# Kernel tuning notes

Measured on AMD Instinct MI355X. Metric: run time of the kernel, lower is better.

Reference implementation:

```python
import jax, jax.numpy as jnp
import numpy as np

DIM = 4096
N_HEADS = 32
N_KV = 8
HD = 128
SW = 4096          # sliding window / cache length
B = 32             # max_batch_size (decode batch)
MAX_SEQ = 8192
START_POS = 4000
CURRENT_POS = 4000

def _nearest_32(n):
    return ((n + 31) // 32) * 32

PADDED_LEN = min(_nearest_32(START_POS + 1), SW)  # 4032

def _rope_tables():
    inv_freq = 1.0 / (10000.0 ** (np.arange(0, HD, 2, dtype=np.float32) / HD))
    t = np.arange(MAX_SEQ, dtype=np.float32)
    freqs = np.outer(t, inv_freq)                       # [MAX_SEQ, HD/2]
    emb = np.concatenate([freqs, freqs], axis=-1)       # [MAX_SEQ, HD]
    return jnp.asarray(np.cos(emb)), jnp.asarray(np.sin(emb))

def rotate_half(u):
    u1, u2 = jnp.split(u, 2, axis=-1)
    return jnp.concatenate([-u2, u1], axis=-1)

def setup_inputs() -> dict:
    key = jax.random.key(0)
    ks = jax.random.split(key, 6)
    cos_cached, sin_cached = _rope_tables()
    return {
        "x": jax.random.normal(ks[0], (1, 1, B, DIM), jnp.float32),
        "wqkv": jax.random.normal(ks[1], (DIM, DIM + 2 * N_KV * HD), jnp.float32) * 0.02,
        "wo": jax.random.normal(ks[2], (DIM, DIM), jnp.float32) * 0.02,
        "cache_k": jax.random.normal(ks[3], (B, N_KV, SW, HD), jnp.float32) * 0.5,
        "cache_v": jax.random.normal(ks[4], (B, N_KV, SW, HD), jnp.float32) * 0.5,
        "cos_cached": cos_cached,
        "sin_cached": sin_cached,
        "attn_mask": jnp.zeros((B, N_HEADS, 1, PADDED_LEN), jnp.float32),
        "start_pos": START_POS,
        "current_pos": CURRENT_POS,
    }

def reference(x, wqkv, wo, cache_k, cache_v, cos_cached, sin_cached, attn_mask,
              start_pos, current_pos):
    group = N_HEADS // N_KV
    padded_len = min(_nearest_32(start_pos + 1), SW)
    scale = 1.0 / jnp.sqrt(jnp.float32(HD))

    # fused QKV projection: x (1,1,B,DIM) @ wqkv -> (B, DIM + 2*N_KV*HD)
    xqkv = x[0, 0] @ wqkv
    q = xqkv[:, :DIM].reshape(B, N_HEADS, HD)
    k = xqkv[:, DIM:DIM + N_KV * HD].reshape(B, N_KV, HD)
    v = xqkv[:, DIM + N_KV * HD:].reshape(B, N_KV, HD)

    # rotary embedding at position start_pos (single decode token)
    cos = cos_cached[start_pos]   # [HD]
    sin = sin_cached[start_pos]
    q = q * cos + rotate_half(q) * sin
    k = k * cos + rotate_half(k) * sin

    # sliding-window KV cache update at current_pos
    cache_k = cache_k.at[:, :, current_pos, :].set(k)
    cache_v = cache_v.at[:, :, current_pos, :].set(v)
    keys = cache_k[:, :, :padded_len, :]     # [B, N_KV, L, HD]
    values = cache_v[:, :, :padded_len, :]

    # grouped attention: q heads grouped by kv head
    qg = q.reshape(B, N_KV, group, HD)
    scores = jnp.einsum('bkgd,bkld->bkgl', qg, keys) * scale
    scores = scores + attn_mask.reshape(B, N_KV, group, padded_len)
    probs = jax.nn.softmax(scores, axis=-1)
    out = jnp.einsum('bkgl,bkld->bkgd', probs, values)   # [B, N_KV, group, HD]

    # concat heads and output projection
    dense = out.reshape(B, DIM) @ wo
    return dense.reshape(1, 1, B, DIM)
```

## Files before the change

### kernel.cpp

```cpp
#include <hip/hip_runtime.h>
#include <hip/hip_bf16.h>

typedef unsigned int u32;
typedef unsigned short u16;

__device__ __forceinline__ u16 f2bf(float f){ u32 x; __builtin_memcpy(&x,&f,4); u32 r=(x+0x7fffu+((x>>16)&1u))>>16; return (u16)r; }
__device__ __forceinline__ float lo2f(u32 u){ u32 x=u<<16; float f; __builtin_memcpy(&f,&x,4); return f; }
__device__ __forceinline__ float hi2f(u32 u){ u32 x=u&0xffff0000u; float f; __builtin_memcpy(&f,&x,4); return f; }

__global__ __launch_bounds__(256) void transpose_x(
    const float* __restrict__ x, float* __restrict__ xt)
{
    __shared__ float ld[32][65];
    const int t = threadIdx.x;
    const int g = blockIdx.x;
    #pragma unroll
    for (int i=0;i<8;++i) {
        const int e = i*256 + t;
        const int b = e >> 6, dd = e & 63;
        ld[b][dd] = x[(size_t)b*4096 + g*64 + dd];
    }
    __syncthreads();
    #pragma unroll
    for (int i=0;i<8;++i) {
        const int e = i*256 + t;
        const int dd = e >> 5, b = e & 31;
        xt[(size_t)(g*64 + dd)*32 + b] = ld[b][dd];
    }
}

__global__ __launch_bounds__(256) void gemm_splitk_t(
    const float* __restrict__ At, const float2* __restrict__ W2,
    float* __restrict__ P, int K, int N, int dps)
{
    const int j2 = blockIdx.x*256 + threadIdx.x;
    const int s = blockIdx.y;
    float acc0[32], acc1[32];
    #pragma unroll
    for (int b=0;b<32;++b){ acc0[b]=0.f; acc1[b]=0.f; }
    const int d0 = s*dps, d1 = d0 + dps;
    const int halfN = N >> 1;
    #pragma unroll 2
    for (int d=d0; d<d1; ++d) {
        const float2 wv = W2[(size_t)d*halfN + j2];
        const float* __restrict__ Ad = At + d*32;
        #pragma unroll
        for (int b=0;b<32;++b) {
            const float av = Ad[b];
            acc0[b] = fmaf(av, wv.x, acc0[b]);
            acc1[b] = fmaf(av, wv.y, acc1[b]);
        }
    }
    float* Pp = P + (size_t)(s*32)*N + 2*j2;
    #pragma unroll
    for (int b=0;b<32;++b)
        *reinterpret_cast<float2*>(Pp + (size_t)b*N) = make_float2(acc0[b], acc1[b]);
}

__global__ __launch_bounds__(256) void qkv_finish(
    const float* __restrict__ P, const float* __restrict__ cosc,
    const float* __restrict__ sinc, const int* __restrict__ spp,
    float* __restrict__ qws, float* __restrict__ kn, float* __restrict__ vn,
    int splits)
{
    __shared__ float sh[256];
    const int t = threadIdx.x;
    const int col = blockIdx.x*256 + t;
    const int b = blockIdx.y;
    float v = 0.f;
    for (int s=0;s<splits;++s) v += P[(size_t)(s*32+b)*6144 + col];
    sh[t] = v;
    __syncthreads();
    if (col < 5120) {
        const int d = col & 127;
        const int pt = (t & ~127) | ((d<64)? d+64 : d-64);
        const float pv = sh[pt];
        const int spos = *spp;
        const float c  = cosc[spos*128 + d];
        const float sn = sinc[spos*128 + d];
        const float rot = (d<64)? -pv : pv;
        const float val = fmaf(v, c, rot*sn);
        if (col < 4096) qws[(size_t)b*4096 + col] = val;
        else            kn[(size_t)b*1024 + (col-4096)] = val;
    } else {
        vn[(size_t)b*1024 + (col-5120)] = v;
    }
}

__global__ __launch_bounds__(1024, 4) void attn_kernel(
    const float* __restrict__ qws, const float* __restrict__ Kc,
    const float* __restrict__ Vc, const float* __restrict__ kn,
    const float* __restrict__ vn, const float* __restrict__ mask,
    const int* __restrict__ curp, float* __restrict__ aout_t,
    const int PL, const int SW)
{
    __shared__ float scoresS[4*4100];
    __shared__ float obuf[16][4][128];
    __shared__ float redm[16][4];
    __shared__ float reds[16][4];

    const int t = threadIdx.x;
    const int lane = t & 63;
    const int w = t >> 6;
    const int b  = blockIdx.x >> 3;
    const int kv = blockIdx.x & 7;
    const int cur = *curp;

    const size_t mat = (size_t)(b*8+kv);
    const float* __restrict__ Kb  = Kc + mat*(size_t)SW*128;
    const float* __restrict__ knr = kn + mat*128;
    const float* __restrict__ qbase = qws + (size_t)(b*32 + kv*4)*128;

    const int l   = lane & 15;
    const int grp = lane >> 4;
    float qv[4][8];
    #pragma unroll
    for (int h=0;h<4;++h)
        #pragma unroll
        for (int j=0;j<8;++j)
            qv[h][j] = qbase[h*128 + l*8 + j];

    const int rpw = PL >> 4;
    const int rb0 = w * rpw;
    for (int g=0; g<rpw; g+=4) {
        const int r = rb0 + g + grp;
        const float* __restrict__ row = (r==cur) ? knr : (Kb + (size_t)r*128);
        const float4 ka = *reinterpret_cast<const float4*>(row + l*8);
        const float4 kb4 = *reinterpret_cast<const float4*>(row + l*8 + 4);
        float kf[8];
        kf[0]=ka.x; kf[1]=ka.y; kf[2]=ka.z; kf[3]=ka.w;
        kf[4]=kb4.x; kf[5]=kb4.y; kf[6]=kb4.z; kf[7]=kb4.w;
        float sc0=0.f, sc1=0.f, sc2=0.f, sc3=0.f;
        #pragma unroll
        for (int j=0;j<8;++j) {
            sc0 = fmaf(qv[0][j], kf[j], sc0);
            sc1 = fmaf(qv[1][j], kf[j], sc1);
            sc2 = fmaf(qv[2][j], kf[j], sc2);
            sc3 = fmaf(qv[3][j], kf[j], sc3);
        }
        #pragma unroll
        for (int off=8; off; off>>=1) {
            sc0 += __shfl_xor(sc0, off, 16);
            sc1 += __shfl_xor(sc1, off, 16);
            sc2 += __shfl_xor(sc2, off, 16);
            sc3 += __shfl_xor(sc3, off, 16);
        }
        if (l < 4) {
            const float v = (l==0)?sc0:(l==1)?sc1:(l==2)?sc2:sc3;
            scoresS[l*4100 + r] = v;
        }
    }
    __syncthreads();

    const float scale = 0.08838834764831845f;
    const size_t mbase = ((size_t)b*32 + (size_t)kv*4)*(size_t)PL;
    const float* __restrict__ Vb  = Vc + mat*(size_t)SW*128;
    const float* __restrict__ vnr = vn + mat*128;
    const int chunk = PL >> 4;
    const int p0 = w*chunk, p1 = p0 + chunk;

    float m0=-3.0e38f, m1=-3.0e38f, m2=-3.0e38f, m3=-3.0e38f;
    float l0=0.f, l1=0.f, l2=0.f, l3=0.f;
    float a0[4] = {0.f,0.f,0.f,0.f}, a1[4] = {0.f,0.f,0.f,0.f};

    #pragma unroll 4
    for (int p=p0; p<p1; ++p) {
        const float* row = (p==cur) ? vnr : (Vb + (size_t)p*128);
        const float2 vv = *reinterpret_cast<const float2*>(row + 2*lane);

        const float sc0 = fmaf(scoresS[         p], scale, mask[mbase              + p]);
        const float sc1 = fmaf(scoresS[ 4100 +  p], scale, mask[mbase +   (size_t)PL + p]);
        const float sc2 = fmaf(scoresS[ 8200 +  p], scale, mask[mbase + 2*(size_t)PL + p]);
        const float sc3 = fmaf(scoresS[12300 +  p], scale, mask[mbase + 3*(size_t)PL + p]);

        const float n0 = fmaxf(m0, sc0), n1 = fmaxf(m1, sc1);
        const float n2 = fmaxf(m2, sc2), n3 = fmaxf(m3, sc3);
        const float f0 = __expf(m0 - n0), f1 = __expf(m1 - n1);
        const float f2 = __expf(m2 - n2), f3 = __expf(m3 - n3);
        const float e0 = __expf(sc0 - n0), e1 = __expf(sc1 - n1);
        const float e2 = __expf(sc2 - n2), e3 = __expf(sc3 - n3);
        m0 = n0; m1 = n1; m2 = n2; m3 = n3;
        l0 = fmaf(l0, f0, e0); l1 = fmaf(l1, f1, e1);
        l2 = fmaf(l2, f2, e2); l3 = fmaf(l3, f3, e3);

        a0[0] = fmaf(e0, vv.x, a0[0]*f0); a1[0] = fmaf(e0, vv.y, a1[0]*f0);
        a0[1] = fmaf(e1, vv.x, a0[1]*f1); a1[1] = fmaf(e1, vv.y, a1[1]*f1);
        a0[2] = fmaf(e2, vv.x, a0[2]*f2); a1[2] = fmaf(e2, vv.y, a1[2]*f2);
        a0[3] = fmaf(e3, vv.x, a0[3]*f3); a1[3] = fmaf(e3, vv.y, a1[3]*f3);
    }

    if (lane==0) {
        redm[w][0]=m0; redm[w][1]=m1; redm[w][2]=m2; redm[w][3]=m3;
        reds[w][0]=l0; reds[w][1]=l1; reds[w][2]=l2; reds[w][3]=l3;
    }
    #pragma unroll
    for (int h=0;h<4;++h)
        *reinterpret_cast<float2*>(&obuf[w][h][2*lane]) = make_float2(a0[h], a1[h]);
    __syncthreads();

    if (t < 512) {
        const int h = t >> 7;
        const int d = t & 127;
        float M = redm[0][h];
        #pragma unroll
        for (int ww=1;ww<16;++ww) M = fmaxf(M, redm[ww][h]);
        float num = 0.f, den = 0.f;
        #pragma unroll
        for (int ww=0;ww<16;++ww) {
            const float f = __expf(redm[ww][h] - M);
            num = fmaf(f, obuf[ww][h][d], num);
            den = fmaf(f, reds[ww][h], den);
        }
        const int col = (kv*4 + h)*128 + d;
        aout_t[(size_t)col*32 + b] = num/den;
    }
}

__global__ __launch_bounds__(256) void wo_finish(
    const float* __restrict__ P, float* __restrict__ out, int splits)
{
    const int col = blockIdx.x*256 + threadIdx.x;
    const int b = blockIdx.y;
    float v = 0.f;
    for (int s=0;s<splits;++s) v += P[(size_t)(s*32+b)*4096 + col];
    out[(size_t)b*4096 + col] = v;
}

extern "C" void kernel_launch(void* const* d_in, const int* in_sizes, int n_in,
                              void* d_out, int out_size, void* d_ws, size_t ws_size,
                              hipStream_t stream)
{
    const float* x    = (const float*)d_in[0];
    const float* wqkv = (const float*)d_in[1];
    const float* wo   = (const float*)d_in[2];
    const float* cK   = (const float*)d_in[3];
    const float* cV   = (const float*)d_in[4];
    const float* cosc = (const float*)d_in[5];
    const float* sinc = (const float*)d_in[6];
    const float* mask = (const float*)d_in[7];
    const int* sp   = (const int*)d_in[8];
    const int* cp   = (const int*)d_in[9];

    const int PL = in_sizes[7] / (32*32);
    const int SW = in_sizes[3] / (32*8*128);

    char* ws = (char*)d_ws;
    float* xt    = (float*)(ws);
    float* qws   = (float*)(ws + 524288);
    float* aout_t= (float*)(ws + 2*524288);
    float* kn    = (float*)(ws + 3*524288);
    float* vn    = (float*)(ws + 3*524288 + 131072);
    float* Pbuf  = (float*)(ws + 3*524288 + 2*131072);

    const int splits = 64;
    const int dps = 4096 / splits;

    transpose_x<<<64, 256, 0, stream>>>(x, xt);
    gemm_splitk_t<<<dim3(12, splits), 256, 0, stream>>>(xt, (const float2*)wqkv, Pbuf, 4096, 6144, dps);
    qkv_finish<<<dim3(24, 32), 256, 0, stream>>>(Pbuf, cosc, sinc, sp, qws, kn, vn, splits);

    attn_kernel<<<256, 1024, 0, stream>>>(qws, cK, cV, kn, vn, mask, cp, aout_t, PL, SW);

    gemm_splitk_t<<<dim3(8, splits), 256, 0, stream>>>(aout_t, (const float2*)wo, Pbuf, 4096, 4096, dps);
    wo_finish<<<dim3(16, 32), 256, 0, stream>>>(Pbuf, (float*)d_out, splits);
}
```

Baseline: 329.8 us.

## Compute per-wave max during QK pass and drop online softmax rescaling

Each wave now applies scale and mask while writing scores, tracks a per-head max, and reduces it across the wave. The PV loop then uses that fixed max, removing the per-step rescale exps and multiplies, and the block-wide sync between the two phases. Each lane now handles two rows per step with float4 V loads, and the halves are combined with cross-lane shuffles. The score rows each wave reads are the ones it wrote itself, so dropping the barrier is safe, but it relies on that row ownership staying fixed.

Measured after the change: 314.6 us. 4.6% less time.

```diff
diff --git a/kernel.cpp b/kernel.cpp
--- a/kernel.cpp
+++ b/kernel.cpp
@@ -5,8 +5,6 @@
 typedef unsigned short u16;
 
 __device__ __forceinline__ u16 f2bf(float f){ u32 x; __builtin_memcpy(&x,&f,4); u32 r=(x+0x7fffu+((x>>16)&1u))>>16; return (u16)r; }
-__device__ __forceinline__ float lo2f(u32 u){ u32 x=u<<16; float f; __builtin_memcpy(&f,&x,4); return f; }
-__device__ __forceinline__ float hi2f(u32 u){ u32 x=u&0xffff0000u; float f; __builtin_memcpy(&f,&x,4); return f; }
 
 __global__ __launch_bounds__(256) void transpose_x(
     const float* __restrict__ x, float* __restrict__ xt)
@@ -111,6 +109,9 @@
     const float* __restrict__ knr = kn + mat*128;
     const float* __restrict__ qbase = qws + (size_t)(b*32 + kv*4)*128;
 
+    const float scale = 0.08838834764831845f;
+    const size_t mbase = ((size_t)b*32 + (size_t)kv*4)*(size_t)PL;
+
     const int l   = lane & 15;
     const int grp = lane >> 4;
     float qv[4][8];
@@ -122,6 +123,7 @@
 
     const int rpw = PL >> 4;
     const int rb0 = w * rpw;
+    float mA = -3.0e38f;
     for (int g=0; g<rpw; g+=4) {
         const int r = rb0 + g + grp;
         const float* __restrict__ row = (r==cur) ? knr : (Kb + (size_t)r*128);
@@ -147,55 +149,61 @@
         }
         if (l < 4) {
             const float v = (l==0)?sc0:(l==1)?sc1:(l==2)?sc2:sc3;
-            scoresS[l*4100 + r] = v;
-        }
-    }
-    __syncthreads();
-
-    const float scale = 0.08838834764831845f;
-    const size_t mbase = ((size_t)b*32 + (size_t)kv*4)*(size_t)PL;
+            const float mv = mask[mbase + (size_t)l*PL + r];
+            const float sv = fmaf(v, scale, mv);
+            scoresS[l*4100 + r] = sv;
+            mA = fmaxf(mA, sv);
+        }
+    }
+    mA = fmaxf(mA, __shfl_xor(mA, 16, 64));
+    mA = fmaxf(mA, __shfl_xor(mA, 32, 64));
+    const float m0 = __shfl(mA, 0, 64);
+    const float m1 = __shfl(mA, 1, 64);
+    const float m2 = __shfl(mA, 2, 64);
+    const float m3 = __shfl(mA, 3, 64);
+
     const float* __restrict__ Vb  = Vc + mat*(size_t)SW*128;
     const float* __restrict__ vnr = vn + mat*128;
-    const int chunk = PL >> 4;
-    const int p0 = w*chunk, p1 = p0 + chunk;
-
-    float m0=-3.0e38f, m1=-3.0e38f, m2=-3.0e38f, m3=-3.0e38f;
+    const int dl = lane & 31;
+    const int pr = lane >> 5;
+    const int p0 = rb0, p1 = rb0 + rpw;
     float l0=0.f, l1=0.f, l2=0.f, l3=0.f;
-    float a0[4] = {0.f,0.f,0.f,0.f}, a1[4] = {0.f,0.f,0.f,0.f};
-
+    float4 A0 = make_float4(0.f,0.f,0.f,0.f);
+    float4 A1 = make_float4(0.f,0.f,0.f,0.f);
+    float4 A2 = make_float4(0.f,0.f,0.f,0.f);
+    float4 A3 = make_float4(0.f,0.f,0.f,0.f);
     #pragma unroll 4
-    for (int p=p0; p<p1; ++p) {
-        const float* row = (p==cur) ? vnr : (Vb + (size_t)p*128);
-        const float2 vv = *reinterpret_cast<const float2*>(row + 2*lane);
-
-        const float sc0 = fmaf(scoresS[         p], scale, mask[mbase              + p]);
-        const float sc1 = fmaf(scoresS[ 4100 +  p], scale, mask[mbase +   (size_t)PL + p]);
-        const float sc2 = fmaf(scoresS[ 8200 +  p], scale, mask[mbase + 2*(size_t)PL + p]);
-        const float sc3 = fmaf(scoresS[12300 +  p], scale, mask[mbase + 3*(size_t)PL + p]);
-
-        const float n0 = fmaxf(m0, sc0), n1 = fmaxf(m1, sc1);
-        const float n2 = fmaxf(m2, sc2), n3 = fmaxf(m3, sc3);
-        const float f0 = __expf(m0 - n0), f1 = __expf(m1 - n1);
-        const float f2 = __expf(m2 - n2), f3 = __expf(m3 - n3);
-        const float e0 = __expf(sc0 - n0), e1 = __expf(sc1 - n1);
-        const float e2 = __expf(sc2 - n2), e3 = __expf(sc3 - n3);
-        m0 = n0; m1 = n1; m2 = n2; m3 = n3;
-        l0 = fmaf(l0, f0, e0); l1 = fmaf(l1, f1, e1);
-        l2 = fmaf(l2, f2, e2); l3 = fmaf(l3, f3, e3);
-
-        a0[0] = fmaf(e0, vv.x, a0[0]*f0); a1[0] = fmaf(e0, vv.y, a1[0]*f0);
-        a0[1] = fmaf(e1, vv.x, a0[1]*f1); a1[1] = fmaf(e1, vv.y, a1[1]*f1);
-        a0[2] = fmaf(e2, vv.x, a0[2]*f2); a1[2] = fmaf(e2, vv.y, a1[2]*f2);
-        a0[3] = fmaf(e3, vv.x, a0[3]*f3); a1[3] = fmaf(e3, vv.y, a1[3]*f3);
-    }
+    for (int p=p0; p<p1; p+=2) {
+        const int pp = p + pr;
+        const float* row = (pp==cur) ? vnr : (Vb + (size_t)pp*128);
+        const float4 vv = *reinterpret_cast<const float4*>(row + 4*dl);
+        const float e0 = __expf(scoresS[         pp] - m0);
+        const float e1 = __expf(scoresS[ 4100 +  pp] - m1);
+        const float e2 = __expf(scoresS[ 8200 +  pp] - m2);
+        const float e3 = __expf(scoresS[12300 +  pp] - m3);
+        l0 += e0; l1 += e1; l2 += e2; l3 += e3;
+        A0.x=fmaf(e0,vv.x,A0.x); A0.y=fmaf(e0,vv.y,A0.y); A0.z=fmaf(e0,vv.z,A0.z); A0.w=fmaf(e0,vv.w,A0.w);
+        A1.x=fmaf(e1,vv.x,A1.x); A1.y=fmaf(e1,vv.y,A1.y); A1.z=fmaf(e1,vv.z,A1.z); A1.w=fmaf(e1,vv.w,A1.w);
+        A2.x=fmaf(e2,vv.x,A2.x); A2.y=fmaf(e2,vv.y,A2.y); A2.z=fmaf(e2,vv.z,A2.z); A2.w=fmaf(e2,vv.w,A2.w);
+        A3.x=fmaf(e3,vv.x,A3.x); A3.y=fmaf(e3,vv.y,A3.y); A3.z=fmaf(e3,vv.z,A3.z); A3.w=fmaf(e3,vv.w,A3.w);
+    }
+    A0.x+=__shfl_xor(A0.x,32,64); A0.y+=__shfl_xor(A0.y,32,64); A0.z+=__shfl_xor(A0.z,32,64); A0.w+=__shfl_xor(A0.w,32,64);
+    A1.x+=__shfl_xor(A1.x,32,64); A1.y+=__shfl_xor(A1.y,32,64); A1.z+=__shfl_xor(A1.z,32,64); A1.w+=__shfl_xor(A1.w,32,64);
+    A2.x+=__shfl_xor(A2.x,32,64); A2.y+=__shfl_xor(A2.y,32,64); A2.z+=__shfl_xor(A2.z,32,64); A2.w+=__shfl_xor(A2.w,32,64);
+    A3.x+=__shfl_xor(A3.x,32,64); A3.y+=__shfl_xor(A3.y,32,64); A3.z+=__shfl_xor(A3.z,32,64); A3.w+=__shfl_xor(A3.w,32,64);
+    l0 += __shfl_xor(l0,32,64); l1 += __shfl_xor(l1,32,64);
+    l2 += __shfl_xor(l2,32,64); l3 += __shfl_xor(l3,32,64);
 
     if (lane==0) {
         redm[w][0]=m0; redm[w][1]=m1; redm[w][2]=m2; redm[w][3]=m3;
         reds[w][0]=l0; reds[w][1]=l1; reds[w][2]=l2; reds[w][3]=l3;
     }
-    #pragma unroll
-    for (int h=0;h<4;++h)
-        *reinterpret_cast<float2*>(&obuf[w][h][2*lane]) = make_float2(a0[h], a1[h]);
+    if (pr==0) {
+        *reinterpret_cast<float4*>(&obuf[w][0][4*dl]) = A0;
+        *reinterpret_cast<float4*>(&obuf[w][1][4*dl]) = A1;
+        *reinterpret_cast<float4*>(&obuf[w][2][4*dl]) = A2;
+        *reinterpret_cast<float4*>(&obuf[w][3][4*dl]) = A3;
+    }
     __syncthreads();
 
     if (t < 512) {
```
